# Performance work log

Measured on AMD Instinct MI355X. Metric: run time of the kernel, lower is better.

Reference implementation:

```python
import jax, jax.numpy as jnp
import numpy as np

VOCAB, EMBED, SEQ, HID = 50000, 128, 200, 30
BATCH = 4096


def setup_inputs() -> dict:
    key = jax.random.key(0)
    ks = jax.random.split(key, 14)
    s = lambda fan_in: 1.0 / np.sqrt(fan_in)
    return {
        "tokens": jax.random.randint(ks[0], (BATCH, SEQ), 0, VOCAB, dtype=jnp.int32),
        "emb": jax.random.normal(ks[1], (VOCAB, EMBED), jnp.float32) * 0.05,
        "Wx": jax.random.normal(ks[2], (EMBED, HID), jnp.float32) * s(EMBED),
        "Wh": jax.random.normal(ks[3], (HID, HID), jnp.float32) * s(HID),
        "b_rnn": jnp.zeros((HID,), jnp.float32),
        "W1": jax.random.normal(ks[4], (HID, 128), jnp.float32) * s(HID),
        "b1": jnp.zeros((128,), jnp.float32),
        "W2": jax.random.normal(ks[5], (128, 64), jnp.float32) * s(128),
        "b2": jnp.zeros((64,), jnp.float32),
        "W3": jax.random.normal(ks[6], (64, 32), jnp.float32) * s(64),
        "b3": jnp.zeros((32,), jnp.float32),
        "Wo": jax.random.normal(ks[7], (32, 1), jnp.float32) * s(32),
        "bo": jnp.zeros((1,), jnp.float32),
    }


def reference(tokens, emb, Wx, Wh, b_rnn, W1, b1, W2, b2, W3, b3, Wo, bo):
    # Embedding lookup: [B, T, E]
    x = emb[tokens]
    # SimpleRNN (tanh), return last hidden state. Precompute input projection
    # once as a big GEMM, then scan the recurrence over time.
    xp = jnp.einsum("bte,eh->tbh", x, Wx) + b_rnn  # [T, B, H]
    h0 = jnp.zeros((tokens.shape[0], Wh.shape[0]), x.dtype)

    def step(h, xp_t):
        h_new = jnp.tanh(xp_t + h @ Wh)
        return h_new, None

    h_last, _ = jax.lax.scan(step, h0, xp)
    # Dense head (dropout layers are identity at inference).
    d1 = jax.nn.relu(h_last @ W1 + b1)
    d2 = jax.nn.relu(d1 @ W2 + b2)
    d3 = jax.nn.relu(d2 @ W3 + b3)
    return jax.nn.sigmoid(d3 @ Wo + bo)
```

## Files before the change

kernel.cpp:

```cpp
#include <hip/hip_runtime.h>
#include <math.h>

#define VOCAB 50000
#define EMBED 128
#define SEQ   200
#define HID   30
#define BATCH 4096

typedef float4 __attribute__((__may_alias__)) f4ma;

__device__ __forceinline__ float tanh_fast(float x) {
    float e = __expf(2.0f * x);
    return 1.0f - __fdividef(2.0f, e + 1.0f);
}
__device__ __forceinline__ float swz16_f(float x) {
    return __int_as_float(__builtin_amdgcn_ds_swizzle(__float_as_int(x), 0x401F));
}

__global__ __launch_bounds__(256, 2) void embproj_kernel(
    const float* __restrict__ emb, const float* __restrict__ Wx,
    const float* __restrict__ brnn, float* __restrict__ embP)
{
    int tid  = threadIdx.x;
    int wv   = tid >> 6;
    int l    = tid & 63;
    int j16  = l & 15;
    int p    = (l >> 4) & 1;
    int g    = l >> 5;
    int col  = j16 + 16 * g;
    int colc = (col < HID) ? col : (HID - 1);
    int k0   = 64 * p;

    float whx[64];
    #pragma unroll
    for (int i = 0; i < 64; ++i)
        whx[i] = Wx[(k0 + i) * HID + colc];
    float bj = brnn[colc];

    int base = (blockIdx.x * 4 + wv) * 25;

    float4 eA[16], eB[16];
    #define LOADROW(dst, v) { \
        int vc = min((v), VOCAB - 1); \
        const f4ma* e4 = (const f4ma*)(emb + (size_t)vc * EMBED + k0); \
        _Pragma("unroll") \
        for (int q = 0; q < 16; ++q) dst[q] = e4[q]; \
    }
    #define COMPUTE(src, v) { \
        float a0 = 0.f, a1 = 0.f, a2 = 0.f, a3 = 0.f; \
        _Pragma("unroll") \
        for (int q = 0; q < 16; ++q) { \
            a0 += src[q].x * whx[4*q+0]; \
            a1 += src[q].y * whx[4*q+1]; \
            a2 += src[q].z * whx[4*q+2]; \
            a3 += src[q].w * whx[4*q+3]; \
        } \
        float own  = (a0 + a1) + (a2 + a3); \
        float full = bj + (own + swz16_f(own)); \
        if (p == 0 && col < HID && (v) < VOCAB) \
            embP[(size_t)(v) * HID + col] = full; \
    }

    LOADROW(eA, base + 0);
    for (int r = 0; r < 25; r += 2) {
        LOADROW(eB, base + r + 1);
        COMPUTE(eA, base + r);
        LOADROW(eA, base + r + 2);
        COMPUTE(eB, base + r + 1);
    }
    #undef LOADROW
    #undef COMPUTE
}

__global__ __launch_bounds__(256, 2) void rnn_head_kernel(
    const int* __restrict__ tokens, const float* __restrict__ embP,
    const float* __restrict__ Wh,
    const float* __restrict__ W1, const float* __restrict__ b1,
    const float* __restrict__ W2, const float* __restrict__ b2,
    const float* __restrict__ W3, const float* __restrict__ b3,
    const float* __restrict__ Wo, const float* __restrict__ bo,
    float* __restrict__ out)
{
    __shared__ __align__(16) float hL[8][32];
    __shared__ float d1L[8][128];
    __shared__ float d2L[8][64];

    int tid  = threadIdx.x;
    int wv   = tid >> 6;
    int l    = tid & 63;
    int half = l >> 5;
    int j    = l & 31;
    int j16  = l & 15;
    int p    = (l >> 4) & 1;
    int rloc = wv * 2 + half;
    int b    = blockIdx.x * 8 + rloc;

    const int* trow = tokens + (size_t)b * SEQ;
    int jc = (j < HID) ? j : (HID - 1);

    hL[rloc][j] = 0.0f;
    __builtin_amdgcn_sched_barrier(0);

    int cB = j16 + 16;
    float whA[16], whB[16];
    #pragma unroll
    for (int kk = 0; kk < 16; ++kk) {
        int k = 16 * p + kk;
        whA[kk] = (k < HID) ? Wh[k * HID + j16] : 0.0f;
        whB[kk] = (k < HID && cB < HID) ? Wh[k * HID + cB] : 0.0f;
    }

    float xq[8]; int tr[8];
    #pragma unroll
    for (int s = 0; s < 8; ++s) {
        xq[s] = embP[(size_t)trow[s] * HID + jc];
        tr[s] = trow[8 + s];
    }

    for (int t = 0; t < SEQ; t += 8) {
        #pragma unroll
        for (int s = 0; s < 8; ++s) {
            float hv[16];
            const f4ma* h4 = (const f4ma*)(&hL[rloc][16 * p]);
            #pragma unroll
            for (int qq = 0; qq < 4; ++qq) {
                f4ma hh = h4[qq];
                hv[4*qq+0] = hh.x; hv[4*qq+1] = hh.y;
                hv[4*qq+2] = hh.z; hv[4*qq+3] = hh.w;
            }
            float xp = xq[s];
            xq[s] = embP[(size_t)tr[s] * HID + jc];
            int tn = t + 16 + s; tn = (tn < SEQ) ? tn : SEQ - 1;
            tr[s] = trow[tn];

            float a0=0.f, a1=0.f, b0=0.f, b1=0.f;
            #pragma unroll
            for (int kk = 0; kk < 16; kk += 2) {
                a0 += hv[kk]   * whA[kk];
                a1 += hv[kk+1] * whA[kk+1];
                b0 += hv[kk]   * whB[kk];
                b1 += hv[kk+1] * whB[kk+1];
            }
            float pA = a0 + a1;
            float pB = b0 + b1;
            float own  = p ? pB : pA;
            float send = p ? pA : pB;
            float recv = swz16_f(send);
            float hn = tanh_fast(xp + (own + recv));
            if (j < HID) hL[rloc][j] = hn;
            __builtin_amdgcn_sched_barrier(0);
        }
    }

    {
        #pragma unroll
        for (int qq = 0; qq < 4; ++qq) {
            int c = j + 32 * qq;
            float acc = b1[c];
            #pragma unroll
            for (int k = 0; k < HID; ++k) acc += hL[rloc][k] * W1[k * 128 + c];
            d1L[rloc][c] = fmaxf(acc, 0.0f);
        }
        #pragma unroll
        for (int qq = 0; qq < 2; ++qq) {
            int c = j + 32 * qq;
            float acc = b2[c];
            #pragma unroll 8
            for (int k = 0; k < 128; ++k) acc += d1L[rloc][k] * W2[k * 64 + c];
            d2L[rloc][c] = fmaxf(acc, 0.0f);
        }
        float acc3 = b3[j];
        #pragma unroll 8
        for (int k = 0; k < 64; ++k) acc3 += d2L[rloc][k] * W3[k * 32 + j];
        acc3 = fmaxf(acc3, 0.0f);
        float prod = acc3 * Wo[j];
        #pragma unroll
        for (int m = 16; m > 0; m >>= 1) prod += __shfl_xor(prod, m, 32);
        if (j == 0) out[b] = 1.0f / (1.0f + __expf(-(prod + bo[0])));
    }
}

extern "C" void kernel_launch(void* const* d_in, const int* in_sizes, int n_in,
                              void* d_out, int out_size, void* d_ws, size_t ws_size,
                              hipStream_t stream) {
    (void)in_sizes; (void)n_in; (void)out_size; (void)ws_size;
    const int*   tokens = (const int*)  d_in[0];
    const float* emb    = (const float*)d_in[1];
    const float* Wx     = (const float*)d_in[2];
    const float* Wh     = (const float*)d_in[3];
    const float* brnn   = (const float*)d_in[4];
    const float* W1     = (const float*)d_in[5];
    const float* b1     = (const float*)d_in[6];
    const float* W2     = (const float*)d_in[7];
    const float* b2     = (const float*)d_in[8];
    const float* W3     = (const float*)d_in[9];
    const float* b3     = (const float*)d_in[10];
    const float* Wo     = (const float*)d_in[11];
    const float* bo     = (const float*)d_in[12];
    float* out  = (float*)d_out;
    float* embP = (float*)d_ws;

    embproj_kernel<<<512, 256, 0, stream>>>(emb, Wx, brnn, embP);
    rnn_head_kernel<<<BATCH / 8, 256, 0, stream>>>(
        tokens, embP, Wh, W1, b1, W2, b2, W3, b3, Wo, bo, out);
}
```

Before: 95.56 us.

## Remap RNN lanes so cross-half exchange uses permlane32 swap, smaller blocks

Reorganizes the recurrence lane mapping so the two 16-lane halves of each hidden-state row sit in opposite 32-lane halves of the wave. The partial dot-product exchange then uses the permlane32_swap builtin instead of an LDS-backed ds_swizzle. Blocks shrink from 256 threads covering 8 rows to 128 threads covering 4 rows, with the dense head remapped to match. The aim is lower latency on the serial per-timestep critical path, at the cost of a runtime lane-selection check and more, smaller blocks.

Result: no change. 95.74 us (median of 2 runs) (+0.2%).

```diff
diff --git a/kernel.cpp b/kernel.cpp
--- a/kernel.cpp
+++ b/kernel.cpp
@@ -8,6 +8,7 @@
 #define BATCH 4096
 
 typedef float4 __attribute__((__may_alias__)) f4ma;
+typedef unsigned int uint2v __attribute__((ext_vector_type(2)));
 
 __device__ __forceinline__ float tanh_fast(float x) {
     float e = __expf(2.0f * x);
@@ -72,7 +73,7 @@
     #undef COMPUTE
 }
 
-__global__ __launch_bounds__(256, 2) void rnn_head_kernel(
+__global__ __launch_bounds__(128) void rnn_head_kernel(
     const int* __restrict__ tokens, const float* __restrict__ embP,
     const float* __restrict__ Wh,
     const float* __restrict__ W1, const float* __restrict__ b1,
@@ -81,25 +82,32 @@
     const float* __restrict__ Wo, const float* __restrict__ bo,
     float* __restrict__ out)
 {
-    __shared__ __align__(16) float hL[8][32];
-    __shared__ float d1L[8][128];
-    __shared__ float d2L[8][64];
+    __shared__ __align__(16) float hL[4][32];
+    __shared__ float d1L[4][128];
+    __shared__ float d2L[4][64];
 
     int tid  = threadIdx.x;
     int wv   = tid >> 6;
     int l    = tid & 63;
-    int half = l >> 5;
-    int j    = l & 31;
     int j16  = l & 15;
-    int p    = (l >> 4) & 1;
-    int rloc = wv * 2 + half;
-    int b    = blockIdx.x * 8 + rloc;
+    int row  = (l >> 4) & 1;
+    int p    = l >> 5;
+    int j    = j16 + 16 * p;
+    int rloc = wv * 2 + row;
+    int b    = blockIdx.x * 4 + rloc;
 
     const int* trow = tokens + (size_t)b * SEQ;
     int jc = (j < HID) ? j : (HID - 1);
 
     hL[rloc][j] = 0.0f;
     __builtin_amdgcn_sched_barrier(0);
+
+    bool useR0;
+    {
+        unsigned li = (unsigned)l;
+        uint2v rp = __builtin_amdgcn_permlane32_swap(li, li, false, false);
+        useR0 = (rp[0] == (unsigned)(l ^ 32));
+    }
 
     int cB = j16 + 16;
     float whA[16], whB[16];
@@ -145,7 +153,9 @@
             float pB = b0 + b1;
             float own  = p ? pB : pA;
             float send = p ? pA : pB;
-            float recv = swz16_f(send);
+            unsigned si = __float_as_uint(send);
+            uint2v sw = __builtin_amdgcn_permlane32_swap(si, si, false, false);
+            float recv = __uint_as_float(useR0 ? sw[0] : sw[1]);
             float hn = tanh_fast(xp + (own + recv));
             if (j < HID) hL[rloc][j] = hn;
             __builtin_amdgcn_sched_barrier(0);
@@ -153,30 +163,33 @@
     }
 
     {
+        int half = l >> 5, j32 = l & 31;
+        int rh = wv * 2 + half;
+        int bB = blockIdx.x * 4 + rh;
         #pragma unroll
         for (int qq = 0; qq < 4; ++qq) {
-            int c = j + 32 * qq;
+            int c = j32 + 32 * qq;
             float acc = b1[c];
             #pragma unroll
-            for (int k = 0; k < HID; ++k) acc += hL[rloc][k] * W1[k * 128 + c];
-            d1L[rloc][c] = fmaxf(acc, 0.0f);
+            for (int k = 0; k < HID; ++k) acc += hL[rh][k] * W1[k * 128 + c];
+            d1L[rh][c] = fmaxf(acc, 0.0f);
         }
         #pragma unroll
         for (int qq = 0; qq < 2; ++qq) {
-            int c = j + 32 * qq;
+            int c = j32 + 32 * qq;
             float acc = b2[c];
             #pragma unroll 8
-            for (int k = 0; k < 128; ++k) acc += d1L[rloc][k] * W2[k * 64 + c];
-            d2L[rloc][c] = fmaxf(acc, 0.0f);
+            for (int k = 0; k < 128; ++k) acc += d1L[rh][k] * W2[k * 64 + c];
+            d2L[rh][c] = fmaxf(acc, 0.0f);
         }
-        float acc3 = b3[j];
+        float acc3 = b3[j32];
         #pragma unroll 8
-        for (int k = 0; k < 64; ++k) acc3 += d2L[rloc][k] * W3[k * 32 + j];
+        for (int k = 0; k < 64; ++k) acc3 += d2L[rh][k] * W3[k * 32 + j32];
         acc3 = fmaxf(acc3, 0.0f);
-        float prod = acc3 * Wo[j];
+        float prod = acc3 * Wo[j32];
         #pragma unroll
         for (int m = 16; m > 0; m >>= 1) prod += __shfl_xor(prod, m, 32);
-        if (j == 0) out[b] = 1.0f / (1.0f + __expf(-(prod + bo[0])));
+        if (j32 == 0) out[bB] = 1.0f / (1.0f + __expf(-(prod + bo[0])));
     }
 }
 
@@ -201,6 +214,6 @@
     float* embP = (float*)d_ws;
 
     embproj_kernel<<<512, 256, 0, stream>>>(emb, Wx, brnn, embP);
-    rnn_head_kernel<<<BATCH / 8, 256, 0, stream>>>(
+    rnn_head_kernel<<<BATCH / 4, 128, 0, stream>>>(
         tokens, embP, Wh, W1, b1, W2, b2, W3, b3, Wo, bo, out);
 }
```
